# Kernel optimization log

Hardware: AMD Instinct MI355X
Metric: run time of the kernel (lower is better)

Reference implementation:

```python
import jax, jax.numpy as jnp
import numpy as np


def _conv(x, w, b, pad):
    y = jax.lax.conv_general_dilated(
        x, w, window_strides=(1, 1), padding=[(pad, pad), (pad, pad)],
        dimension_numbers=('NCHW', 'OIHW', 'NCHW'))
    return y + b[None, :, None, None]


def _grid_sample(img, gxn, gyn):
    # img [N,C,H,W]; gxn,gyn [N,H,W] normalized coords.
    # Matches torch grid_sample(mode='bilinear', padding_mode='zeros', align_corners=False).
    N, C, H, W = img.shape
    ix = ((gxn + 1.0) * W - 1.0) * 0.5
    iy = ((gyn + 1.0) * H - 1.0) * 0.5
    ix0 = jnp.floor(ix); iy0 = jnp.floor(iy)
    ix1 = ix0 + 1.0; iy1 = iy0 + 1.0
    wx1 = ix - ix0; wy1 = iy - iy0
    wx0 = 1.0 - wx1; wy0 = 1.0 - wy1
    bidx = jnp.arange(N)[:, None, None]

    def gather(yy, xx):
        valid = (xx >= 0) & (xx < W) & (yy >= 0) & (yy < H)
        xc = jnp.clip(xx, 0, W - 1).astype(jnp.int32)
        yc = jnp.clip(yy, 0, H - 1).astype(jnp.int32)
        v = img[bidx, :, yc, xc]  # [N,H,W,C]
        return jnp.where(valid[..., None], v, jnp.zeros((), img.dtype))

    out = (gather(iy0, ix0) * (wy0 * wx0)[..., None]
           + gather(iy0, ix1) * (wy0 * wx1)[..., None]
           + gather(iy1, ix0) * (wy1 * wx0)[..., None]
           + gather(iy1, ix1) * (wy1 * wx1)[..., None])
    return jnp.transpose(out, (0, 3, 1, 2))  # [N,C,H,W]


def reference(inputs, state, i2h_w, i2h_b, i2f_w, i2f_b, h2f_w, h2f_b,
              flows_w, flows_b, wrap_w, wrap_b):
    B, T, Cin, H, W = inputs.shape
    hid = state.shape[1]
    L = flows_w.shape[0] // 2

    # input-to-hidden for all timesteps at once (as in the torch code)
    i2h = _conv(inputs.reshape(B * T, Cin, H, W), i2h_w, i2h_b, 1)
    i2h = i2h.reshape(B, T, 3 * hid, H, W)
    r_i, u_i, n_i = jnp.split(i2h, 3, axis=2)

    gx, gy = jnp.meshgrid(jnp.arange(W, dtype=inputs.dtype),
                          jnp.arange(H, dtype=inputs.dtype))  # each [H,W]

    def step(h, xs):
        x_t, r_t, u_t, n_t = xs
        f = jnp.tanh(_conv(x_t, i2f_w, i2f_b, 2) + _conv(h, h2f_w, h2f_b, 2))
        flows = _conv(f, flows_w, flows_b, 2).reshape(B, L, 2, H, W)
        # vgrid = grid + (-flow), then normalize by 2*v/size - 1
        vx = gx[None, None] - flows[:, :, 0]
        vy = gy[None, None] - flows[:, :, 1]
        gxn = 2.0 * vx / W - 1.0
        gyn = 2.0 * vy / H - 1.0
        img = jnp.broadcast_to(h[:, None], (B, L, hid, H, W)).reshape(B * L, hid, H, W)
        warped = _grid_sample(img, gxn.reshape(B * L, H, W), gyn.reshape(B * L, H, W))
        warped = warped.reshape(B, L * hid, H, W)
        h2h = _conv(warped, wrap_w, wrap_b, 0)
        r_h, u_h, n_h = jnp.split(h2h, 3, axis=1)
        r = jax.nn.sigmoid(r_t + r_h)
        u = jax.nn.sigmoid(u_t + u_h)
        n = jax.nn.sigmoid(n_t + r * n_h)  # note: sigmoid, faithful to source
        h_new = (1.0 - u) * n + u * h
        return h_new, h_new

    xs = (jnp.swapaxes(inputs, 0, 1),
          jnp.swapaxes(r_i, 0, 1),
          jnp.swapaxes(u_i, 0, 1),
          jnp.swapaxes(n_i, 0, 1))
    h_last, outs = jax.lax.scan(step, state, xs)
    outputs = jnp.swapaxes(outs, 0, 1)  # [B,T,hid,H,W]
    return outputs, h_last


def setup_inputs() -> dict:
    key = jax.random.key(0)
    ks = jax.random.split(key, 8)
    B, T, Cin, H, W = 4, 10, 8, 96, 96
    hid, L = 64, 13

    def w(k, shape):
        fan_in = int(np.prod(shape[1:]))
        return jax.random.normal(k, shape, jnp.float32) * (1.0 / np.sqrt(fan_in))

    return {
        'inputs': jax.random.normal(ks[0], (B, T, Cin, H, W), jnp.float32),
        'state': jnp.zeros((B, hid, H, W), jnp.float32),
        'i2h_w': w(ks[1], (3 * hid, Cin, 3, 3)), 'i2h_b': jnp.zeros((3 * hid,), jnp.float32),
        'i2f_w': w(ks[2], (32, Cin, 5, 5)), 'i2f_b': jnp.zeros((32,), jnp.float32),
        'h2f_w': w(ks[3], (32, hid, 5, 5)), 'h2f_b': jnp.zeros((32,), jnp.float32),
        'flows_w': w(ks[4], (2 * L, 32, 5, 5)), 'flows_b': jnp.zeros((2 * L,), jnp.float32),
        'wrap_w': w(ks[5], (3 * hid, hid * L, 1, 1)), 'wrap_b': jnp.zeros((3 * hid,), jnp.float32),
    }
```

## Files before the change

kernel.cpp:

```cpp
#include <hip/hip_runtime.h>
#include <math.h>

#define HW 9216

typedef __attribute__((ext_vector_type(8))) short short8;
typedef __attribute__((ext_vector_type(4))) float float4v;

__device__ __forceinline__ float sigmoidf_(float x) { return 1.0f / (1.0f + expf(-x)); }

__device__ __forceinline__ short bf16rne(float f) {
  unsigned u = __builtin_bit_cast(unsigned, f);
  unsigned r = (u + 0x7FFFu + ((u >> 16) & 1u)) >> 16;
  return (short)r;
}
__device__ __forceinline__ float bf2f(short s) {
  return __builtin_bit_cast(float, ((unsigned)(unsigned short)s) << 16);
}

__global__ __launch_bounds__(256) void k_wconv(const float* __restrict__ w,
                                               short* __restrict__ o)
{
  int i = blockIdx.x * 256 + threadIdx.x;
  if (i >= 192 * 832) return;
  int n = i / 832, k = i % 832;
  int l = k >> 6, c = k & 63;
  o[((size_t)l * 192 + n) * 64 + c] = bf16rne(w[i]);
}

__global__ __launch_bounds__(256) void k_pack(
    const float* __restrict__ wh, const float* __restrict__ wi,
    const float* __restrict__ flw,
    short* __restrict__ whK, short* __restrict__ wiK, short* __restrict__ flK)
{
  int i = blockIdx.x * 256 + threadIdx.x;
  if (i < 51200) {
    int t = i / 2048, rem = i % 2048;
    int o = rem / 64, c = rem % 64;
    whK[i] = bf16rne(wh[((size_t)(o * 64 + c)) * 25 + t]);
  } else if (i < 58368) {
    int j = i - 51200;
    int g = j / 1024, rem = j % 1024;
    int o = rem / 32, k = rem % 32;
    int q = k / 8, ch = k % 8;
    int tap = g * 4 + q;
    wiK[j] = (tap < 25) ? bf16rne(wi[((size_t)(o * 8 + ch)) * 25 + tap]) : (short)0;
  } else {
    int j = i - 58368;
    int t = j / 1024, rem = j % 1024;
    int o = rem / 32, c = rem % 32;
    flK[j] = (o < 26) ? bf16rne(flw[((size_t)(o * 32 + c)) * 25 + t]) : (short)0;
  }
}

__global__ __launch_bounds__(256) void k_h2bf(const float* __restrict__ st,
                                              short* __restrict__ hbf)
{
  const int tid = threadIdx.x;
  const int pp = tid & 63, cg = tid >> 6;
  const int b = blockIdx.y;
  const int p = blockIdx.x * 64 + pp;
  short s[16];
  #pragma unroll
  for (int k = 0; k < 16; ++k)
    s[k] = bf16rne(st[((size_t)b * 64 + cg * 16 + k) * HW + p]);
  short* dst = hbf + ((size_t)b * HW + p) * 64 + cg * 16;
  *(short8*)dst = *(short8*)&s[0];
  *(short8*)(dst + 8) = *(short8*)&s[8];
}

__global__ __launch_bounds__(256) void k_x2bf(const float* __restrict__ inp,
                                              short* __restrict__ xbf)
{
  const int p  = blockIdx.x * 256 + threadIdx.x;
  const int bt = blockIdx.y;
  short s[8];
  #pragma unroll
  for (int ci = 0; ci < 8; ++ci)
    s[ci] = bf16rne(inp[((size_t)bt * 8 + ci) * HW + p]);
  *(short8*)(xbf + ((size_t)bt * HW + p) * 8) = *(short8*)s;
}

__global__ __launch_bounds__(256) void k_i2h(
    const float* __restrict__ inp, int t_off,
    const float* __restrict__ w, const float* __restrict__ bias,
    short* __restrict__ out)
{
  const int p  = blockIdx.x * 256 + threadIdx.x;
  const int og = blockIdx.y;
  const int zz = blockIdx.z;
  const int t  = zz >> 2, b = zz & 3;
  const int y = p / 96, x = p % 96;
  const float* xin = inp + ((size_t)(b * 10 + t + t_off)) * 8 * HW;
  float acc[4];
  #pragma unroll
  for (int i = 0; i < 4; ++i) acc[i] = bias[og * 4 + i];
  for (int ci = 0; ci < 8; ++ci) {
    const float* xc = xin + (size_t)ci * HW;
    float v[9];
    #pragma unroll
    for (int ky = 0; ky < 3; ++ky) {
      int yy = y + ky - 1;
      bool vy = (yy >= 0) && (yy < 96);
      #pragma unroll
      for (int kx = 0; kx < 3; ++kx) {
        int xx = x + kx - 1;
        bool ok = vy && (xx >= 0) && (xx < 96);
        v[ky * 3 + kx] = ok ? xc[yy * 96 + xx] : 0.0f;
      }
    }
    #pragma unroll
    for (int i = 0; i < 4; ++i) {
      const float* wc = w + (((size_t)(og * 4 + i)) * 8 + ci) * 9;
      #pragma unroll
      for (int k = 0; k < 9; ++k) acc[i] += wc[k] * v[k];
    }
  }
  #pragma unroll
  for (int i = 0; i < 4; ++i)
    out[((size_t)(zz * 192 + og * 4 + i)) * HW + p] = bf16rne(acc[i]);
}

__global__ __launch_bounds__(256) void k_f(
    const short* __restrict__ xbf, int t,
    const short* __restrict__ hbf,
    const short* __restrict__ whK,
    const short* __restrict__ wiK,
    const float* __restrict__ bi, const float* __restrict__ bh,
    short* __restrict__ fbf)
{
  const int tid = threadIdx.x;
  const int lane = tid & 63;
  const int w = tid >> 6;
  const int ml = lane & 15, qd = lane >> 4;
  const int b = blockIdx.y;
  const int px0 = blockIdx.x * 64 + w * 16;
  const int y0 = px0 / 96, xc0 = px0 % 96;
  const int xcol = xc0 + ml;
  const int px = px0 + ml;
  const short* hb = hbf + (size_t)b * HW * 64;
  const short* xb = xbf + ((size_t)(b * 10 + t)) * HW * 8;

  float4v acc0 = {0.f, 0.f, 0.f, 0.f};
  float4v acc1 = {0.f, 0.f, 0.f, 0.f};

  #pragma unroll
  for (int ky = 0; ky < 5; ++ky) {
    int yy = y0 + ky - 2;
    if (yy < 0 || yy >= 96) continue;
    #pragma unroll
    for (int kx = 0; kx < 5; ++kx) {
      int xx = xcol + kx - 2;
      bool cv = (xx >= 0) && (xx < 96);
      int off = (ky - 2) * 96 + (kx - 2);
      const short* ap = hb + (size_t)(px + off) * 64 + qd * 8;
      short8 a0 = {}, a1 = {};
      if (cv) { a0 = *(const short8*)ap; a1 = *(const short8*)(ap + 32); }
      int tap = ky * 5 + kx;
      const short* bp = whK + ((size_t)tap * 32 + ml) * 64 + qd * 8;
      short8 b00 = *(const short8*)bp;
      short8 b01 = *(const short8*)(bp + 32);
      short8 b10 = *(const short8*)(bp + 16 * 64);
      short8 b11 = *(const short8*)(bp + 16 * 64 + 32);
      acc0 = __builtin_amdgcn_mfma_f32_16x16x32_bf16(a0, b00, acc0, 0, 0, 0);
      acc0 = __builtin_amdgcn_mfma_f32_16x16x32_bf16(a1, b01, acc0, 0, 0, 0);
      acc1 = __builtin_amdgcn_mfma_f32_16x16x32_bf16(a0, b10, acc1, 0, 0, 0);
      acc1 = __builtin_amdgcn_mfma_f32_16x16x32_bf16(a1, b11, acc1, 0, 0, 0);
    }
  }

  #pragma unroll
  for (int g = 0; g < 7; ++g) {
    int tap = g * 4 + qd;
    int dy = tap / 5 - 2;
    int dx = tap - (dy + 2) * 5 - 2;
    int yy = y0 + dy, xx = xcol + dx;
    bool v = (tap < 25) && (yy >= 0) && (yy < 96) && (xx >= 0) && (xx < 96);
    short8 a = {};
    if (v) a = *(const short8*)(xb + (size_t)(px + dy * 96 + dx) * 8);
    const short* bp = wiK + ((size_t)g * 32 + ml) * 32 + qd * 8;
    short8 b0 = *(const short8*)bp;
    short8 b1 = *(const short8*)(bp + 16 * 32);
    acc0 = __builtin_amdgcn_mfma_f32_16x16x32_bf16(a, b0, acc0, 0, 0, 0);
    acc1 = __builtin_amdgcn_mfma_f32_16x16x32_bf16(a, b1, acc1, 0, 0, 0);
  }

  short* fo = fbf + (size_t)b * HW * 32;
  #pragma unroll
  for (int i = 0; i < 2; ++i) {
    int o = i * 16 + ml;
    float bias = bi[o] + bh[o];
    float4v a = i ? acc1 : acc0;
    #pragma unroll
    for (int r = 0; r < 4; ++r) {
      int p2 = px0 + qd * 4 + r;
      fo[(size_t)p2 * 32 + o] = bf16rne(tanhf(a[r] + bias));
    }
  }
}

__global__ __launch_bounds__(256) void k_flows(
    const short* __restrict__ fbf,
    const short* __restrict__ flK,
    const float* __restrict__ bias,
    float* __restrict__ fls)
{
  const int tid = threadIdx.x;
  const int lane = tid & 63;
  const int w = tid >> 6;
  const int ml = lane & 15, qd = lane >> 4;
  const int b = blockIdx.y;
  const int px0 = blockIdx.x * 64 + w * 16;
  const int y0 = px0 / 96, xc0 = px0 % 96;
  const int xcol = xc0 + ml;
  const int px = px0 + ml;
  const short* fb = fbf + (size_t)b * HW * 32;

  float4v acc0 = {0.f, 0.f, 0.f, 0.f};
  float4v acc1 = {0.f, 0.f, 0.f, 0.f};

  #pragma unroll
  for (int ky = 0; ky < 5; ++ky) {
    int yy = y0 + ky - 2;
    if (yy < 0 || yy >= 96) continue;
    #pragma unroll
    for (int kx = 0; kx < 5; ++kx) {
      int xx = xcol + kx - 2;
      bool cv = (xx >= 0) && (xx < 96);
      int off = (ky - 2) * 96 + (kx - 2);
      short8 a = {};
      if (cv) a = *(const short8*)(fb + (size_t)(px + off) * 32 + qd * 8);
      int tap = ky * 5 + kx;
      const short* bp = flK + ((size_t)tap * 32 + ml) * 32 + qd * 8;
      short8 b0 = *(const short8*)bp;
      short8 b1 = *(const short8*)(bp + 16 * 32);
      acc0 = __builtin_amdgcn_mfma_f32_16x16x32_bf16(a, b0, acc0, 0, 0, 0);
      acc1 = __builtin_amdgcn_mfma_f32_16x16x32_bf16(a, b1, acc1, 0, 0, 0);
    }
  }

  float* fo = fls + (size_t)b * 26 * HW;
  #pragma unroll
  for (int i = 0; i < 2; ++i) {
    int o = i * 16 + ml;
    if (o < 26) {
      float bv = bias[o];
      float4v a = i ? acc1 : acc0;
      #pragma unroll
      for (int r = 0; r < 4; ++r)
        fo[(size_t)o * HW + px0 + qd * 4 + r] = a[r] + bv;
    }
  }
}

__global__ __launch_bounds__(256) void k_fused(
    const float* __restrict__ fls,
    const float* __restrict__ hbase, long long hstr,
    const short* __restrict__ hbf_in,
    const short* __restrict__ i2h,
    const short* __restrict__ wbf,
    const float* __restrict__ wb,
    float* __restrict__ outb, long long ostr,
    short* __restrict__ hbf_out,
    float* __restrict__ lastb)
{
  __shared__ __align__(16) char smem_raw[49920];
  short* lds_w = (short*)smem_raw;
  short* lds_v = lds_w + 192 * 72;
  float* lds_h = (float*)smem_raw;
  short* hpack = (short*)smem_raw;

  const int tid = threadIdx.x;
  const int pp  = tid & 63;
  const int cg  = tid >> 6;
  const int ii  = blockIdx.x;
  const int xcd = ii & 7;
  const int b   = xcd >> 1;
  const int tile = ((ii >> 3) << 1) | (xcd & 1);
  const int p   = tile * 64 + pp;
  const int ypix = p / 96, xpix = p % 96;
  const float* hb  = hbase + (size_t)b * hstr;
  const short* hvp = hbf_in + ((size_t)b * HW) * 64 + cg * 16;
  const float* flb = fls + (size_t)b * 26 * HW;
  const int ml = pp & 15;
  const int qd = pp >> 4;

  float4v acc[3][4];
  #pragma unroll
  for (int i = 0; i < 3; ++i)
    #pragma unroll
    for (int j = 0; j < 4; ++j)
      #pragma unroll
      for (int r = 0; r < 4; ++r) acc[i][j][r] = 0.0f;

  for (int l = 0; l < 13; ++l) {
    __syncthreads();
    {
      const short* wsrc = wbf + (size_t)l * 192 * 64;
      #pragma unroll
      for (int it = 0; it < 6; ++it) {
        int idx = tid + it * 256;
        int n = idx >> 3, c8 = (idx & 7) * 8;
        short8 v = *(const short8*)(wsrc + n * 64 + c8);
        *(short8*)(lds_w + n * 72 + c8) = v;
      }
    }
    float fx = flb[(size_t)(2 * l) * HW + p];
    float fy = flb[(size_t)(2 * l + 1) * HW + p];
    float vx = (float)xpix - fx;
    float vy = (float)ypix - fy;
    float gxn = 2.0f * vx / 96.0f - 1.0f;
    float gyn = 2.0f * vy / 96.0f - 1.0f;
    float ix = ((gxn + 1.0f) * 96.0f - 1.0f) * 0.5f;
    float iy = ((gyn + 1.0f) * 96.0f - 1.0f) * 0.5f;
    float x0f = floorf(ix), y0f = floorf(iy);
    float wx1 = ix - x0f, wy1 = iy - y0f;
    float wx0 = 1.0f - wx1, wy0 = 1.0f - wy1;
    int x0 = (int)x0f, y0 = (int)y0f;
    bool vx0 = (x0 >= 0) && (x0 < 96);
    bool vx1 = (x0 + 1 >= 0) && (x0 + 1 < 96);
    bool vy0g = (y0 >= 0) && (y0 < 96);
    bool vy1g = (y0 + 1 >= 0) && (y0 + 1 < 96);
    int o00 = (vx0 && vy0g) ? (y0 * 96 + x0)           : -1;
    int o01 = (vx1 && vy0g) ? (y0 * 96 + x0 + 1)       : -1;
    int o10 = (vx0 && vy1g) ? ((y0 + 1) * 96 + x0)     : -1;
    int o11 = (vx1 && vy1g) ? ((y0 + 1) * 96 + x0 + 1) : -1;
    float w00 = wy0 * wx0, w01 = wy0 * wx1, w10 = wy1 * wx0, w11 = wy1 * wx1;

    float sum[16];
    #pragma unroll
    for (int k = 0; k < 16; ++k) sum[k] = 0.0f;
    #define TAP_(off, wgt)                                            \
      if ((off) >= 0) {                                               \
        const short* tp = hvp + (size_t)(off) * 64;                   \
        short8 u0 = *(const short8*)tp;                               \
        short8 u1 = *(const short8*)(tp + 8);                         \
        _Pragma("unroll")                                             \
        for (int k = 0; k < 8; ++k) {                                 \
          sum[k]     += (wgt) * bf2f(u0[k]);                          \
          sum[k + 8] += (wgt) * bf2f(u1[k]);                          \
        }                                                             \
      }
    TAP_(o00, w00) TAP_(o01, w01) TAP_(o10, w10) TAP_(o11, w11)
    #undef TAP_
    short vv[16];
    #pragma unroll
    for (int k = 0; k < 16; ++k) vv[k] = bf16rne(sum[k]);
    *(short8*)(lds_v + pp * 72 + cg * 16)     = *(short8*)&vv[0];
    *(short8*)(lds_v + pp * 72 + cg * 16 + 8) = *(short8*)&vv[8];
    __syncthreads();

    #pragma unroll
    for (int ks = 0; ks < 2; ++ks) {
      short8 af[3], bfr[4];
      #pragma unroll
      for (int i = 0; i < 3; ++i)
        af[i] = *(const short8*)(lds_w + (48 * cg + i * 16 + ml) * 72 + ks * 32 + qd * 8);
      #pragma unroll
      for (int j = 0; j < 4; ++j)
        bfr[j] = *(const short8*)(lds_v + (j * 16 + ml) * 72 + ks * 32 + qd * 8);
      #pragma unroll
      for (int i = 0; i < 3; ++i)
        #pragma unroll
        for (int j = 0; j < 4; ++j)
          acc[i][j] = __builtin_amdgcn_mfma_f32_16x16x32_bf16(af[i], bfr[j], acc[i][j], 0, 0, 0);
    }
  }

  __syncthreads();
  #pragma unroll
  for (int i = 0; i < 3; ++i)
    #pragma unroll
    for (int j = 0; j < 4; ++j)
      #pragma unroll
      for (int r = 0; r < 4; ++r) {
        int ch = 48 * cg + i * 16 + qd * 4 + r;
        int px = j * 16 + ml;
        lds_h[ch * 65 + px] = acc[i][j][r];
      }
  __syncthreads();

  const short* i2hb = i2h + (size_t)b * 192 * HW + p;
  float* ob = outb + (size_t)b * ostr;
  float hnv[16];
  #pragma unroll
  for (int k = 0; k < 16; ++k) {
    int cch = cg + k * 4;
    float rh = lds_h[cch * 65 + pp] + wb[cch];
    float uh = lds_h[(64 + cch) * 65 + pp] + wb[64 + cch];
    float nh = lds_h[(128 + cch) * 65 + pp] + wb[128 + cch];
    float rt = bf2f(i2hb[(size_t)cch * HW]);
    float ut = bf2f(i2hb[(size_t)(64 + cch) * HW]);
    float nt = bf2f(i2hb[(size_t)(128 + cch) * HW]);
    float rr = sigmoidf_(rt + rh);
    float uu = sigmoidf_(ut + uh);
    float nn = sigmoidf_(nt + rr * nh);
    float hp = hb[(size_t)cch * HW + p];
    float hn = (1.0f - uu) * nn + uu * hp;
    ob[(size_t)cch * HW + p] = hn;
    if (lastb) lastb[((size_t)b * 64 + cch) * HW + p] = hn;
    hnv[k] = hn;
  }

  __syncthreads();
  #pragma unroll
  for (int k = 0; k < 16; ++k)
    hpack[pp * 80 + cg + 4 * k] = bf16rne(hnv[k]);
  __syncthreads();
  {
    int px = tid >> 2, g = tid & 3;
    short8 a0 = *(short8*)(hpack + px * 80 + g * 16);
    short8 a1 = *(short8*)(hpack + px * 80 + g * 16 + 8);
    short* dst = hbf_out + ((size_t)b * HW + tile * 64 + px) * 64 + g * 16;
    *(short8*)dst = a0;
    *(short8*)(dst + 8) = a1;
  }
}

extern "C" void kernel_launch(void* const* d_in, const int* in_sizes, int n_in,
                              void* d_out, int out_size, void* d_ws, size_t ws_size,
                              hipStream_t stream)
{
  const float* inp   = (const float*)d_in[0];
  const float* state = (const float*)d_in[1];
  const float* i2h_w = (const float*)d_in[2];
  const float* i2h_b = (const float*)d_in[3];
  const float* i2f_w = (const float*)d_in[4];
  const float* i2f_b = (const float*)d_in[5];
  const float* h2f_w = (const float*)d_in[6];
  const float* h2f_b = (const float*)d_in[7];
  const float* fl_w  = (const float*)d_in[8];
  const float* fl_b  = (const float*)d_in[9];
  const float* wr_w  = (const float*)d_in[10];
  const float* wr_b  = (const float*)d_in[11];
  float* out = (float*)d_out;
  float* ws  = (float*)d_ws;

  const long long F_I2HB1 = 3538944;
  const long long F_FBF   = 589824;
  const long long F_FLS   = 958464;
  const long long F_HB    = 1179648;
  const long long F_XBF   = 1474560;
  const long long F_WBF   = 79872;
  const long long F_WHK   = 25600;
  const long long F_WIK   = 3584;
  const long long F_FLK   = 12800;
  const long long OB      = (long long)10 * 64 * HW;

  const long long fixed = F_FBF + F_FLS + 2 * F_HB + F_XBF + F_WBF
                        + F_WHK + F_WIK + F_FLK;
  bool batched = ws_size >= (size_t)(10 * F_I2HB1 + fixed) * 4ULL;
  long long i2h_fl = batched ? 10 * F_I2HB1 : F_I2HB1;

  short* ws_i2h = (short*)ws;
  float* fwp    = ws + i2h_fl;
  float* ws_fbf_f = fwp;              fwp += F_FBF;
  float* ws_fls   = fwp;              fwp += F_FLS;
  float* hbfA_f   = fwp;              fwp += F_HB;
  float* hbfB_f   = fwp;              fwp += F_HB;
  float* xbf_f    = fwp;              fwp += F_XBF;
  float* wbf_f    = fwp;              fwp += F_WBF;
  float* whK_f    = fwp;              fwp += F_WHK;
  float* wiK_f    = fwp;              fwp += F_WIK;
  float* flK_f    = fwp;
  short* ws_fbf = (short*)ws_fbf_f;
  short* hbfA   = (short*)hbfA_f;
  short* hbfB   = (short*)hbfB_f;
  short* ws_xbf = (short*)xbf_f;
  short* ws_wbf = (short*)wbf_f;
  short* ws_whK = (short*)whK_f;
  short* ws_wiK = (short*)wiK_f;
  short* ws_flK = (short*)flK_f;

  k_wconv<<<dim3(624), 256, 0, stream>>>(wr_w, ws_wbf);
  k_pack<<<dim3(328), 256, 0, stream>>>(h2f_w, i2f_w, fl_w, ws_whK, ws_wiK, ws_flK);
  k_h2bf<<<dim3(144, 4), 256, 0, stream>>>(state, hbfA);
  k_x2bf<<<dim3(36, 40), 256, 0, stream>>>(inp, ws_xbf);
  if (batched)
    k_i2h<<<dim3(36, 48, 40), 256, 0, stream>>>(inp, 0, i2h_w, i2h_b, ws_i2h);

  for (int t = 0; t < 10; ++t) {
    const float* hbase = (t == 0) ? state : (out + (size_t)(t - 1) * 64 * HW);
    long long hstr = (t == 0) ? (long long)64 * HW : OB;
    short* hin  = (t & 1) ? hbfB : hbfA;
    short* hout = (t & 1) ? hbfA : hbfB;

    if (!batched)
      k_i2h<<<dim3(36, 48, 4), 256, 0, stream>>>(inp, t, i2h_w, i2h_b, ws_i2h);
    k_f<<<dim3(144, 4), 256, 0, stream>>>(ws_xbf, t, hin, ws_whK, ws_wiK,
                                          i2f_b, h2f_b, ws_fbf);
    k_flows<<<dim3(144, 4), 256, 0, stream>>>(ws_fbf, ws_flK, fl_b, ws_fls);

    const short* i2h_t = batched ? (ws_i2h + (size_t)t * 2 * F_I2HB1) : ws_i2h;
    float* outbase = out + (size_t)t * 64 * HW;
    float* lastb = (t == 9) ? (out + (size_t)4 * 10 * 64 * HW) : nullptr;
    k_fused<<<dim3(576), 256, 0, stream>>>(ws_fls, hbase, hstr, hin, i2h_t,
                                           ws_wbf, wr_b, outbase, OB, hout, lastb);
  }
}
```

Baseline: 1.700 ms.

## Rewrite i2h 3x3 conv as bf16 MFMA implicit GEMM on packed inputs

The input-to-hidden 3x3 convolution moves from a scalar fp32 direct conv to an implicit GEMM. It uses bf16 MFMA 16x16x32 instructions over the already-converted bf16 input and a newly packed weight layout, with taps grouped four per K-slice. Weights are packed in the existing pack kernel. The goal is to cut the ALU cost of the batched precompute, at the price of bf16 rounding of inputs and weights and some zero-padded K work.

```diff
diff --git a/kernel.cpp b/kernel.cpp
--- a/kernel.cpp
+++ b/kernel.cpp
@@ -4,6 +4,7 @@
 #define HW 9216
 
 typedef __attribute__((ext_vector_type(8))) short short8;
+typedef __attribute__((ext_vector_type(4))) short short4v;
 typedef __attribute__((ext_vector_type(4))) float float4v;
 
 __device__ __forceinline__ float sigmoidf_(float x) { return 1.0f / (1.0f + expf(-x)); }
@@ -29,8 +30,9 @@
 
 __global__ __launch_bounds__(256) void k_pack(
     const float* __restrict__ wh, const float* __restrict__ wi,
-    const float* __restrict__ flw,
-    short* __restrict__ whK, short* __restrict__ wiK, short* __restrict__ flK)
+    const float* __restrict__ flw, const float* __restrict__ wih,
+    short* __restrict__ whK, short* __restrict__ wiK, short* __restrict__ flK,
+    short* __restrict__ i2hK)
 {
   int i = blockIdx.x * 256 + threadIdx.x;
   if (i < 51200) {
@@ -44,11 +46,18 @@
     int q = k / 8, ch = k % 8;
     int tap = g * 4 + q;
     wiK[j] = (tap < 25) ? bf16rne(wi[((size_t)(o * 8 + ch)) * 25 + tap]) : (short)0;
-  } else {
+  } else if (i < 83968) {
     int j = i - 58368;
     int t = j / 1024, rem = j % 1024;
     int o = rem / 32, c = rem % 32;
     flK[j] = (o < 26) ? bf16rne(flw[((size_t)(o * 32 + c)) * 25 + t]) : (short)0;
+  } else {
+    int j = i - 83968;
+    int g = j / 6144, rem = j % 6144;
+    int n = rem / 32, k = rem % 32;
+    int q = k / 8, ch = k % 8;
+    int tap = g * 4 + q;
+    i2hK[j] = (tap < 9) ? bf16rne(wih[((size_t)(n * 8 + ch)) * 9 + tap]) : (short)0;
   }
 }
 
@@ -81,43 +90,67 @@
 }
 
 __global__ __launch_bounds__(256) void k_i2h(
-    const float* __restrict__ inp, int t_off,
-    const float* __restrict__ w, const float* __restrict__ bias,
+    const short* __restrict__ xbf, int t_off,
+    const short* __restrict__ wK, const float* __restrict__ bias,
     short* __restrict__ out)
 {
-  const int p  = blockIdx.x * 256 + threadIdx.x;
-  const int og = blockIdx.y;
-  const int zz = blockIdx.z;
-  const int t  = zz >> 2, b = zz & 3;
-  const int y = p / 96, x = p % 96;
-  const float* xin = inp + ((size_t)(b * 10 + t + t_off)) * 8 * HW;
-  float acc[4];
-  #pragma unroll
-  for (int i = 0; i < 4; ++i) acc[i] = bias[og * 4 + i];
-  for (int ci = 0; ci < 8; ++ci) {
-    const float* xc = xin + (size_t)ci * HW;
-    float v[9];
-    #pragma unroll
-    for (int ky = 0; ky < 3; ++ky) {
-      int yy = y + ky - 1;
-      bool vy = (yy >= 0) && (yy < 96);
-      #pragma unroll
-      for (int kx = 0; kx < 3; ++kx) {
-        int xx = x + kx - 1;
-        bool ok = vy && (xx >= 0) && (xx < 96);
-        v[ky * 3 + kx] = ok ? xc[yy * 96 + xx] : 0.0f;
-      }
-    }
-    #pragma unroll
-    for (int i = 0; i < 4; ++i) {
-      const float* wc = w + (((size_t)(og * 4 + i)) * 8 + ci) * 9;
-      #pragma unroll
-      for (int k = 0; k < 9; ++k) acc[i] += wc[k] * v[k];
-    }
-  }
-  #pragma unroll
-  for (int i = 0; i < 4; ++i)
-    out[((size_t)(zz * 192 + og * 4 + i)) * HW + p] = bf16rne(acc[i]);
+  const int tid  = threadIdx.x;
+  const int lane = tid & 63;
+  const int w    = tid >> 6;
+  const int ml = lane & 15, qd = lane >> 4;
+  const int zz = blockIdx.y;
+  const int t = (zz >> 2) + t_off, b = zz & 3;
+  const int pw0 = blockIdx.x * 128 + w * 32;
+  const short* xb = xbf + ((size_t)(b * 10 + t)) * HW * 8;
+
+  short8 afr[2][3];
+  #pragma unroll
+  for (int s = 0; s < 2; ++s) {
+    int px0 = pw0 + s * 16;
+    int y0 = px0 / 96, xc0 = px0 % 96;
+    #pragma unroll
+    for (int g = 0; g < 3; ++g) {
+      int tap = g * 4 + qd;
+      int dy = tap / 3 - 1;
+      int dx = tap % 3 - 1;
+      int yy = y0 + dy, xx = xc0 + ml + dx;
+      bool v = (tap < 9) && (yy >= 0) && (yy < 96) && (xx >= 0) && (xx < 96);
+      short8 a = {};
+      if (v) a = *(const short8*)(xb + (size_t)(px0 + ml + dy * 96 + dx) * 8);
+      afr[s][g] = a;
+    }
+  }
+
+  float4v acc[2][12];
+  #pragma unroll
+  for (int s = 0; s < 2; ++s)
+    #pragma unroll
+    for (int j = 0; j < 12; ++j)
+      #pragma unroll
+      for (int r = 0; r < 4; ++r) acc[s][j][r] = 0.0f;
+
+  #pragma unroll
+  for (int j = 0; j < 12; ++j) {
+    #pragma unroll
+    for (int g = 0; g < 3; ++g) {
+      short8 bf = *(const short8*)(wK + ((size_t)(g * 192 + j * 16 + ml)) * 32 + qd * 8);
+      acc[0][j] = __builtin_amdgcn_mfma_f32_16x16x32_bf16(afr[0][g], bf, acc[0][j], 0, 0, 0);
+      acc[1][j] = __builtin_amdgcn_mfma_f32_16x16x32_bf16(afr[1][g], bf, acc[1][j], 0, 0, 0);
+    }
+  }
+
+  #pragma unroll
+  for (int j = 0; j < 12; ++j) {
+    float bv = bias[j * 16 + ml];
+    #pragma unroll
+    for (int s = 0; s < 2; ++s) {
+      short4v o4;
+      #pragma unroll
+      for (int r = 0; r < 4; ++r) o4[r] = bf16rne(acc[s][j][r] + bv);
+      *(short4v*)(out + ((size_t)(zz * 192 + j * 16 + ml)) * HW
+                      + pw0 + s * 16 + qd * 4) = o4;
+    }
+  }
 }
 
 __global__ __launch_bounds__(256) void k_f(
@@ -444,10 +477,11 @@
   const long long F_WHK   = 25600;
   const long long F_WIK   = 3584;
   const long long F_FLK   = 12800;
+  const long long F_I2HK  = 9216;
   const long long OB      = (long long)10 * 64 * HW;
 
   const long long fixed = F_FBF + F_FLS + 2 * F_HB + F_XBF + F_WBF
-                        + F_WHK + F_WIK + F_FLK;
+                        + F_WHK + F_WIK + F_FLK + F_I2HK;
   bool batched = ws_size >= (size_t)(10 * F_I2HB1 + fixed) * 4ULL;
   long long i2h_fl = batched ? 10 * F_I2HB1 : F_I2HB1;
 
@@ -461,22 +495,25 @@
   float* wbf_f    = fwp;              fwp += F_WBF;
   float* whK_f    = fwp;              fwp += F_WHK;
   float* wiK_f    = fwp;              fwp += F_WIK;
-  float* flK_f    = fwp;
-  short* ws_fbf = (short*)ws_fbf_f;
-  short* hbfA   = (short*)hbfA_f;
-  short* hbfB   = (short*)hbfB_f;
-  short* ws_xbf = (short*)xbf_f;
-  short* ws_wbf = (short*)wbf_f;
-  short* ws_whK = (short*)whK_f;
-  short* ws_wiK = (short*)wiK_f;
-  short* ws_flK = (short*)flK_f;
+  float* flK_f    = fwp;              fwp += F_FLK;
+  float* i2hK_f   = fwp;
+  short* ws_fbf  = (short*)ws_fbf_f;
+  short* hbfA    = (short*)hbfA_f;
+  short* hbfB    = (short*)hbfB_f;
+  short* ws_xbf  = (short*)xbf_f;
+  short* ws_wbf  = (short*)wbf_f;
+  short* ws_whK  = (short*)whK_f;
+  short* ws_wiK  = (short*)wiK_f;
+  short* ws_flK  = (short*)flK_f;
+  short* ws_i2hK = (short*)i2hK_f;
 
   k_wconv<<<dim3(624), 256, 0, stream>>>(wr_w, ws_wbf);
-  k_pack<<<dim3(328), 256, 0, stream>>>(h2f_w, i2f_w, fl_w, ws_whK, ws_wiK, ws_flK);
+  k_pack<<<dim3(400), 256, 0, stream>>>(h2f_w, i2f_w, fl_w, i2h_w,
+                                        ws_whK, ws_wiK, ws_flK, ws_i2hK);
   k_h2bf<<<dim3(144, 4), 256, 0, stream>>>(state, hbfA);
   k_x2bf<<<dim3(36, 40), 256, 0, stream>>>(inp, ws_xbf);
   if (batched)
-    k_i2h<<<dim3(36, 48, 40), 256, 0, stream>>>(inp, 0, i2h_w, i2h_b, ws_i2h);
+    k_i2h<<<dim3(72, 40), 256, 0, stream>>>(ws_xbf, 0, ws_i2hK, i2h_b, ws_i2h);
 
   for (int t = 0; t < 10; ++t) {
     const float* hbase = (t == 0) ? state : (out + (size_t)(t - 1) * 64 * HW);
@@ -485,7 +522,7 @@
     short* hout = (t & 1) ? hbfA : hbfB;
 
     if (!batched)
-      k_i2h<<<dim3(36, 48, 4), 256, 0, stream>>>(inp, t, i2h_w, i2h_b, ws_i2h);
+      k_i2h<<<dim3(72, 4), 256, 0, stream>>>(ws_xbf, t, ws_i2hK, i2h_b, ws_i2h);
     k_f<<<dim3(144, 4), 256, 0, stream>>>(ws_xbf, t, hin, ws_whK, ws_wiK,
                                           i2f_b, h2f_b, ws_fbf);
     k_flows<<<dim3(144, 4), 256, 0, stream>>>(ws_fbf, ws_flK, fl_b, ws_fls);
```

Measured after the change: 1.515 ms. -10.9%, faster.
